# Kernel optimization log

Measured on AMD Instinct MI355X. Metric: run time of the kernel, lower is better.

The kernel has to match this reference:

```python
import jax, jax.numpy as jnp
import numpy as np

V, E, H, B, S, T, NE, NC = 50000, 300, 150, 64, 16, 48, 100001, 300


def bigru(x, Wih, Whh, bih, bhh):
    # x: [T, N, D]; PyTorch GRU cell math, bidirectional -> [T, N, 2H]
    outs = []
    for d in range(2):
        def step(h, xt, d=d):
            gi = xt @ Wih[d].T + bih[d]
            gh = h @ Whh[d].T + bhh[d]
            ir, iz, inn = jnp.split(gi, 3, axis=-1)
            hr, hz, hn = jnp.split(gh, 3, axis=-1)
            r = jax.nn.sigmoid(ir + hr)
            z = jax.nn.sigmoid(iz + hz)
            n = jnp.tanh(inn + r * hn)
            h2 = (1.0 - z) * n + z * h
            return h2, h2
        h0 = jnp.zeros((x.shape[1], Whh.shape[-1]), x.dtype)
        _, hs = jax.lax.scan(step, h0, x, reverse=(d == 1))
        outs.append(hs)
    return jnp.concatenate(outs, axis=-1)


def attend(hs, W, b, ctx):
    # hs: [T, N, G]; softmax attention over time axis
    u = jnp.tanh(jnp.einsum('tng,hg->tnh', hs, W) + b)
    a = jax.nn.softmax(jnp.einsum('tnh,h->tn', u, ctx), axis=0)
    return jnp.einsum('tn,tng->ng', a, hs)


def cos_sim(a, c, eps=1e-8):
    # a: [B, D], c: [B, K, D] -> [B, K]  (torch.cosine_similarity semantics)
    num = jnp.einsum('bd,bkd->bk', a, c)
    den = jnp.linalg.norm(a, axis=-1, keepdims=True) * jnp.linalg.norm(c, axis=-1)
    return num / jnp.maximum(den, eps)


def setup_inputs() -> dict:
    key = jax.random.key(0)
    ks = jax.random.split(key, 20)
    nrm = lambda k, s: (jax.random.normal(k, s, jnp.float32) * 0.05)
    return {
        'docs': jax.random.randint(ks[0], (B, S, T), 0, V),
        'sens': jax.random.randint(ks[1], (B,), 0, S),
        'candidates': jax.random.randint(ks[2], (B, 1, NC), 0, NE),
        'idx': jax.random.randint(ks[3], (B,), 1, NC + 1),  # 1-based gold id
        'word_emb': nrm(ks[4], (V, E)),
        'ent_emb': nrm(ks[5], (NE, E)),
        'Wih_w': nrm(ks[6], (2, 3 * H, E)),
        'Whh_w': nrm(ks[7], (2, 3 * H, H)),
        'bih_w': jnp.zeros((2, 3 * H), jnp.float32),
        'bhh_w': jnp.zeros((2, 3 * H), jnp.float32),
        'attW_w': nrm(ks[8], (2 * H, 2 * H)),
        'attb_w': jnp.zeros((2 * H,), jnp.float32),
        'ctx_w': nrm(ks[9], (2 * H,)),
        'Wih_s': nrm(ks[10], (2, 3 * H, 2 * H)),
        'Whh_s': nrm(ks[11], (2, 3 * H, H)),
        'bih_s': jnp.zeros((2, 3 * H), jnp.float32),
        'bhh_s': jnp.zeros((2, 3 * H), jnp.float32),
        'attW_s': nrm(ks[12], (2 * H, 2 * H)),
        'attb_s': jnp.zeros((2 * H,), jnp.float32),
        'ctx_s': nrm(ks[13], (2 * H,)),
        'linW': nrm(ks[14], (NC, 2 * NC)),
        'linb': jnp.zeros((NC,), jnp.float32),
    }


def reference(docs, sens, candidates, idx, word_emb, ent_emb,
              Wih_w, Whh_w, bih_w, bhh_w, attW_w, attb_w, ctx_w,
              Wih_s, Whh_s, bih_s, bhh_s, attW_s, attb_s, ctx_s,
              linW, linb):
    b, s, t = docs.shape
    # ---- word-level encoder over every sentence at once ----
    x = word_emb[docs]                              # [B,S,T,E]
    x = x.transpose(2, 0, 1, 3).reshape(t, b * s, E)  # [T, B*S, E]
    hs = bigru(x, Wih_w, Whh_w, bih_w, bhh_w)       # [T, B*S, 2H]
    sent_vec = attend(hs, attW_w, attb_w, ctx_w)    # [B*S, 2H]
    sent_vec = sent_vec.reshape(b, s, 2 * H)        # output_per_sen.permute(1,0,2)
    output_sen = sent_vec[jnp.arange(b), sens]      # [B, 2H] mention sentence
    # ---- sentence-level encoder ----
    xs = sent_vec.transpose(1, 0, 2)                # [S, B, 2H]
    hss = bigru(xs, Wih_s, Whh_s, bih_s, bhh_s)     # [S, B, 2H]
    output_doc = attend(hss, attW_s, attb_s, ctx_s)  # [B, 2H]
    # ---- batched cosine similarity against candidate entity embeddings ----
    can = ent_emb[candidates[:, 0]]                 # [B, NC, E]
    sim_total = jnp.concatenate([cos_sim(output_sen, can), cos_sim(output_doc, can)], axis=1)  # [B, 2*NC]
    score = sim_total @ linW.T + linb               # [B, NC]
    score_gold = score[jnp.arange(b), idx - 1]      # [B]
    max_index = jnp.argmax(score, axis=1)           # [B]
    return (score_gold, score, max_index)
```

## Files before the change

### kernel.cpp

```cpp
#include <hip/hip_runtime.h>
#include <hip/hip_bf16.h>
#include <math.h>

#define B_  64
#define S_  16
#define T_  48
#define E_  300
#define H_  150
#define G_  300
#define NC_ 300
#define NW_ (B_*S_)
#define RW_ (T_*NW_)
#define RS_ (S_*B_)
#define GST 960

typedef __attribute__((ext_vector_type(8))) short bf16x8;
typedef __attribute__((ext_vector_type(4))) float f32x4;

__device__ __forceinline__ float sigm(float x){ return 1.0f/(1.0f+__expf(-x)); }

__device__ __forceinline__ ushort f2bf_rne(float x){
  uint u = __float_as_uint(x);
  return (ushort)((u + 0x7FFFu + ((u>>16)&1u)) >> 16);
}

__global__ __launch_bounds__(256) void prep_whh_kernel(
    const float* __restrict__ Whh, float* __restrict__ Wblk){
  int idx = blockIdx.x*256 + threadIdx.x;
  if (idx >= 2*38*450*4) return;
  int k  = idx & 3;
  int j  = (idx >> 2) % 450;
  int e4 = (idx >> 2) / 450 % 38;
  int d  = idx / (38*450*4);
  int e  = e4*4 + k;
  Wblk[idx] = (e < 150) ? Whh[((size_t)d*450 + j)*150 + e] : 0.f;
}

__global__ __launch_bounds__(256) void prep_whh_mfma(
    const float* __restrict__ Whh, ushort* __restrict__ Bsh,
    ushort* __restrict__ Bsl){
  int idx = blockIdx.x*256 + threadIdx.x;
  if (idx >= 2*512*160) return;
  int k = idx % 160;
  int j = (idx / 160) % 512;
  int d = idx / (512*160);
  float x = (j < 450 && k < 150) ? Whh[((size_t)d*450 + j)*150 + k] : 0.f;
  ushort hb = f2bf_rne(x);
  Bsh[idx] = hb;
  Bsl[idx] = f2bf_rne(x - __uint_as_float(((uint)hb)<<16));
}

__global__ __launch_bounds__(128) void split_w_gen(
    const float* __restrict__ W, ushort* __restrict__ Whi,
    ushort* __restrict__ Wlo, int R, int C, int Cp){
  int j = blockIdx.x;
  for (int k = threadIdx.x; k < Cp; k += 128){
    float x = (j < R && k < C) ? W[(size_t)j*C + k] : 0.f;
    ushort hb = f2bf_rne(x);
    float hf = __uint_as_float(((uint)hb)<<16);
    Whi[(size_t)j*Cp + k] = hb;
    Wlo[(size_t)j*Cp + k] = f2bf_rne(x - hf);
  }
}

__global__ __launch_bounds__(256) void gi_mfma_v5(
    const int* __restrict__ docs, const float* __restrict__ emb,
    const ushort* __restrict__ Whi, const ushort* __restrict__ Wlo,
    const float* __restrict__ bih, float* __restrict__ gi){
  __shared__ __align__(16) ushort Bhi[2][16*328];
  __shared__ __align__(16) ushort Blo[2][16*328];
  __shared__ __align__(16) float  Cst[64*36];
  __shared__ int toks[64];
  int tid = threadIdx.x;
  int gr0 = blockIdx.x * 64;
  int t  = gr0 >> 10;
  int n0 = gr0 & 1023;
  if (tid < 64) toks[tid] = docs[(n0 + tid)*T_ + t];
  uint4 pb[5];
#pragma unroll
  for (int i=0;i<5;i++){
    int c = tid + i*256;
    int half = (c >= 640) ? 1 : 0; int cc = c - half*640;
    int row = cc/40, o16 = cc - row*40;
    const ushort* src = half ? Wlo : Whi;
    pb[i] = *(const uint4*)&src[(size_t)row*320 + o16*8];
  }
  __syncthreads();
  int w = tid >> 6, L = tid & 63;
  int lrow = L & 15, lseg = L >> 4;
  const float* aptr = emb + (size_t)toks[w*16 + lrow]*300;
  bf16x8 ah[10], al[10];
#pragma unroll
  for (int ks=0; ks<10; ks++){
    int k0 = ks*32 + lseg*8;
    float x[8];
    if (k0 + 8 <= 300){
      float4 v0 = *(const float4*)&aptr[k0];
      float4 v1 = *(const float4*)&aptr[k0+4];
      x[0]=v0.x; x[1]=v0.y; x[2]=v0.z; x[3]=v0.w;
      x[4]=v1.x; x[5]=v1.y; x[6]=v1.z; x[7]=v1.w;
    } else {
#pragma unroll
      for (int u=0;u<8;u++) x[u] = (k0+u < 300) ? aptr[k0+u] : 0.f;
    }
#pragma unroll
    for (int u=0;u<8;u++){
      ushort hb = f2bf_rne(x[u]);
      float lo = x[u] - __uint_as_float(((uint)hb)<<16);
      ah[ks][u] = (short)hb;
      al[ks][u] = (short)f2bf_rne(lo);
    }
  }
#pragma unroll
  for (int i=0;i<5;i++){
    int c = tid + i*256;
    int half = (c >= 640) ? 1 : 0; int cc = c - half*640;
    int row = cc/40, o16 = cc - row*40;
    ushort* dst = half ? Blo[0] : Bhi[0];
    *(uint4*)&dst[row*328 + o16*8] = pb[i];
  }
  __syncthreads();
  int buf = 0;
  int bfb = lrow*328 + lseg*8;
  int rl0 = w*16 + lseg*4;
  f32x4 acc2[2];
  for (int g2 = 0; g2 < 28; ++g2){
#pragma unroll
    for (int q = 0; q < 2; ++q){
      int nt = g2*2 + q;
#pragma unroll
      for (int i=0;i<5;i++){
        int c = tid + i*256;
        int half = (c >= 640) ? 1 : 0; int cc = c - half*640;
        int row = cc/40, o16 = cc - row*40;
        const ushort* src = half ? Wlo : Whi;
        pb[i] = *(const uint4*)&src[(size_t)((nt+1)*16 + row)*320 + o16*8];
      }
      f32x4 acc = {0.f, 0.f, 0.f, 0.f};
#pragma unroll
      for (int ks=0; ks<10; ks++){
        bf16x8 bh = *(const bf16x8*)&Bhi[buf][bfb + ks*32];
        bf16x8 bl = *(const bf16x8*)&Blo[buf][bfb + ks*32];
        acc = __builtin_amdgcn_mfma_f32_16x16x32_bf16(ah[ks], bh, acc, 0, 0, 0);
        acc = __builtin_amdgcn_mfma_f32_16x16x32_bf16(ah[ks], bl, acc, 0, 0, 0);
        acc = __builtin_amdgcn_mfma_f32_16x16x32_bf16(al[ks], bh, acc, 0, 0, 0);
      }
      acc2[q] = acc;
#pragma unroll
      for (int i=0;i<5;i++){
        int c = tid + i*256;
        int half = (c >= 640) ? 1 : 0; int cc = c - half*640;
        int row = cc/40, o16 = cc - row*40;
        ushort* dst = half ? Blo[buf^1] : Bhi[buf^1];
        *(uint4*)&dst[row*328 + o16*8] = pb[i];
      }
      __syncthreads();
      buf ^= 1;
    }
#pragma unroll
    for (int q = 0; q < 2; ++q){
#pragma unroll
      for (int r = 0; r < 4; ++r)
        Cst[(rl0 + r)*36 + q*16 + lrow] = acc2[q][r];
    }
    __syncthreads();
#pragma unroll
    for (int i = 0; i < 2; ++i){
      int idxc = tid + i*256;
      int row = idxc >> 3, c2 = idxc & 7;
      int colb = g2*32 + c2*4;
      float4 v = *(float4*)&Cst[row*36 + c2*4];
      float4 bb = *(const float4*)&bih[colb];
      v.x += bb.x; v.y += bb.y; v.z += bb.z; v.w += bb.w;
      *(float4*)&gi[(size_t)(gr0 + row)*GST + colb] = v;
    }
  }
  {
    f32x4 acc = {0.f, 0.f, 0.f, 0.f};
#pragma unroll
    for (int ks=0; ks<10; ks++){
      bf16x8 bh = *(const bf16x8*)&Bhi[buf][bfb + ks*32];
      bf16x8 bl = *(const bf16x8*)&Blo[buf][bfb + ks*32];
      acc = __builtin_amdgcn_mfma_f32_16x16x32_bf16(ah[ks], bh, acc, 0, 0, 0);
      acc = __builtin_amdgcn_mfma_f32_16x16x32_bf16(ah[ks], bl, acc, 0, 0, 0);
      acc = __builtin_amdgcn_mfma_f32_16x16x32_bf16(al[ks], bh, acc, 0, 0, 0);
    }
    int col = 896 + lrow;
    if (col < 900){
      float bb = bih[col];
#pragma unroll
      for (int r=0;r<4;r++)
        gi[(size_t)(gr0 + rl0 + r)*GST + col] = acc[r] + bb;
    }
  }
}

__global__ __launch_bounds__(256,3) void att_mfma_kernel(
    const float* __restrict__ hs, const ushort* __restrict__ Whi,
    const ushort* __restrict__ Wlo, const float* __restrict__ bias,
    const float* __restrict__ ctx, float* __restrict__ score, int Rtot){
  __shared__ __align__(16) ushort Bhi[2][16*328];
  __shared__ __align__(16) ushort Blo[2][16*328];
  int tid = threadIdx.x;
  int r0 = blockIdx.x * 64;
  uint4 pb[5];
#pragma unroll
  for (int i=0;i<5;i++){
    int c = tid + i*256;
    int half = (c >= 640) ? 1 : 0; int cc = c - half*640;
    int row = cc/40, o16 = cc - row*40;
    const ushort* src = half ? Wlo : Whi;
    pb[i] = *(const uint4*)&src[(size_t)row*320 + o16*8];
  }
  int w = tid >> 6, L = tid & 63;
  int lrow = L & 15, lseg = L >> 4;
  int arow = r0 + w*16 + lrow;
  bool avalid = arow < Rtot;
  const float* aptr = hs + (size_t)(avalid ? arow : 0)*300;
  bf16x8 ah[10], al[10];
#pragma unroll
  for (int ks=0; ks<10; ks++){
    int k0 = ks*32 + lseg*8;
    float x[8];
    if (avalid && k0 + 8 <= 300){
      float4 v0 = *(const float4*)&aptr[k0];
      float4 v1 = *(const float4*)&aptr[k0+4];
      x[0]=v0.x; x[1]=v0.y; x[2]=v0.z; x[3]=v0.w;
      x[4]=v1.x; x[5]=v1.y; x[6]=v1.z; x[7]=v1.w;
    } else {
#pragma unroll
      for (int u=0;u<8;u++) x[u] = (avalid && k0+u < 300) ? aptr[k0+u] : 0.f;
    }
#pragma unroll
    for (int u=0;u<8;u++){
      ushort hb = f2bf_rne(x[u]);
      float lo = x[u] - __uint_as_float(((uint)hb)<<16);
      ah[ks][u] = (short)hb;
      al[ks][u] = (short)f2bf_rne(lo);
    }
  }
#pragma unroll
  for (int i=0;i<5;i++){
    int c = tid + i*256;
    int half = (c >= 640) ? 1 : 0; int cc = c - half*640;
    int row = cc/40, o16 = cc - row*40;
    ushort* dst = half ? Blo[0] : Bhi[0];
    *(uint4*)&dst[row*328 + o16*8] = pb[i];
  }
  __syncthreads();
  int buf = 0;
  int bfb = lrow*328 + lseg*8;
  float part[4] = {0.f,0.f,0.f,0.f};
  for (int nt = 0; nt < 19; ++nt){
    if (nt < 18){
#pragma unroll
      for (int i=0;i<5;i++){
        int c = tid + i*256;
        int half = (c >= 640) ? 1 : 0; int cc = c - half*640;
        int row = cc/40, o16 = cc - row*40;
        const ushort* src = half ? Wlo : Whi;
        pb[i] = *(const uint4*)&src[(size_t)((nt+1)*16 + row)*320 + o16*8];
      }
    }
    f32x4 acc = {0.f, 0.f, 0.f, 0.f};
#pragma unroll
    for (int ks=0; ks<10; ks++){
      bf16x8 bh = *(const bf16x8*)&Bhi[buf][bfb + ks*32];
      bf16x8 bl = *(const bf16x8*)&Blo[buf][bfb + ks*32];
      acc = __builtin_amdgcn_mfma_f32_16x16x32_bf16(ah[ks], bh, acc, 0, 0, 0);
      acc = __builtin_amdgcn_mfma_f32_16x16x32_bf16(ah[ks], bl, acc, 0, 0, 0);
      acc = __builtin_amdgcn_mfma_f32_16x16x32_bf16(al[ks], bh, acc, 0, 0, 0);
    }
    int col = nt*16 + lrow;
    if (col < 300){
      float bb = bias[col], cx = ctx[col];
#pragma unroll
      for (int r=0;r<4;r++) part[r] += cx * tanhf(acc[r] + bb);
    }
    if (nt < 18){
#pragma unroll
      for (int i=0;i<5;i++){
        int c = tid + i*256;
        int half = (c >= 640) ? 1 : 0; int cc = c - half*640;
        int row = cc/40, o16 = cc - row*40;
        ushort* dst = half ? Blo[buf^1] : Bhi[buf^1];
        *(uint4*)&dst[row*328 + o16*8] = pb[i];
      }
    }
    __syncthreads();
    buf ^= 1;
  }
#pragma unroll
  for (int off=1; off<16; off<<=1){
#pragma unroll
    for (int r=0;r<4;r++) part[r] += __shfl_xor(part[r], off);
  }
  if (lrow == 0){
    int rbase = r0 + w*16 + lseg*4;
#pragma unroll
    for (int r=0;r<4;r++)
      if (rbase + r < Rtot) score[rbase + r] = part[r];
  }
}

__global__ __launch_bounds__(256) void sent_gi_kernel(
    const float* __restrict__ sv, const float* __restrict__ Wih,
    const float* __restrict__ bih, float* __restrict__ gi){
  __shared__ float A[16][G_];
  int r0 = blockIdx.x * 16;
  int s  = r0 >> 6;
  int bb_ = r0 & 63;
  for (int idx = threadIdx.x; idx < 16*75; idx += 256){
    int row = idx / 75, e4 = idx - row*75;
    *(float4*)&A[row][e4*4] =
        *(const float4*)&sv[(((size_t)(bb_+row))*S_ + s)*G_ + e4*4];
  }
  __syncthreads();
  int q = threadIdx.x;
  if (q >= 225) return;
  int j0 = q*4;
  const float4* w0 = (const float4*)(Wih + (size_t)(j0  )*G_);
  const float4* w1 = (const float4*)(Wih + (size_t)(j0+1)*G_);
  const float4* w2 = (const float4*)(Wih + (size_t)(j0+2)*G_);
  const float4* w3 = (const float4*)(Wih + (size_t)(j0+3)*G_);
  float acc[16][4];
#pragma unroll
  for (int i=0;i<16;i++){ acc[i][0]=0.f; acc[i][1]=0.f; acc[i][2]=0.f; acc[i][3]=0.f; }
  for (int e4=0; e4<75; e4++){
    float4 b0=w0[e4], b1=w1[e4], b2=w2[e4], b3=w3[e4];
#pragma unroll
    for (int i=0;i<16;i++){
      float4 av = *(const float4*)&A[i][e4*4];
      acc[i][0] += av.x*b0.x + av.y*b0.y + av.z*b0.z + av.w*b0.w;
      acc[i][1] += av.x*b1.x + av.y*b1.y + av.z*b1.z + av.w*b1.w;
      acc[i][2] += av.x*b2.x + av.y*b2.y + av.z*b2.z + av.w*b2.w;
      acc[i][3] += av.x*b3.x + av.y*b3.y + av.z*b3.z + av.w*b3.w;
    }
  }
  float4 bb = *(const float4*)&bih[j0];
#pragma unroll
  for (int i=0;i<16;i++){
    float4 o4;
    o4.x = acc[i][0]+bb.x; o4.y = acc[i][1]+bb.y;
    o4.z = acc[i][2]+bb.z; o4.w = acc[i][3]+bb.w;
    *(float4*)&gi[((size_t)(s*B_) + bb_ + i)*GST + j0] = o4;
  }
}

__global__ __launch_bounds__(512,2) void gru_mfma2(
    const float* __restrict__ gi, const ushort* __restrict__ Bsh,
    const ushort* __restrict__ Bsl, const float* __restrict__ bhh,
    float* __restrict__ hs, int T, int N){
  __shared__ __align__(16) ushort Ahi[16*168];
  __shared__ __align__(16) ushort Alo[16*168];
  __shared__ float gh[16*468];
  __shared__ float lds_pad[10240];
  int tid = threadIdx.x;
  int d  = blockIdx.y;
  int n0 = blockIdx.x * 8;
  if (N == -12345) lds_pad[tid] = 0.f;
  for (int i = tid; i < 16*168; i += 512){ Ahi[i] = 0; Alo[i] = 0; }
  int wv = tid >> 6, L = tid & 63;
  int lrow = L & 15, lseg = L >> 4;
  bf16x8 Bh[4][5], Bl[4][5];
  {
    const ushort* bh_ = Bsh + (size_t)d*512*160;
    const ushort* bl_ = Bsl + (size_t)d*512*160;
#pragma unroll
    for (int q=0;q<4;q++){
      int row = (wv + q*8)*16 + lrow;
#pragma unroll
      for (int ks=0;ks<5;ks++){
        Bh[q][ks] = *(const bf16x8*)&bh_[(size_t)row*160 + lseg*8 + ks*32];
        Bl[q][ks] = *(const bf16x8*)&bl_[(size_t)row*160 + lseg*8 + ks*32];
      }
    }
  }
  int erow[3], eh[3];
  float bb_r[3], bb_z[3], bb_n[3], hold[3];
#pragma unroll
  for (int r=0;r<3;r++){
    int e = tid + r*512;
    bool v = e < 1200;
    int e2 = v ? e : 0;
    erow[r] = e2 / 150; eh[r] = e2 % 150;
    bb_r[r] = v ? bhh[d*450 + eh[r]]        : 0.f;
    bb_z[r] = v ? bhh[d*450 + 150 + eh[r]]  : 0.f;
    bb_n[r] = v ? bhh[d*450 + 300 + eh[r]]  : 0.f;
    hold[r] = 0.f;
  }
  __syncthreads();
  for (int step = 0; step < T; ++step){
    int t = d ? (T-1-step) : step;
    bf16x8 Ah[5], Al[5];
#pragma unroll
    for (int ks=0;ks<5;ks++){
      Ah[ks] = *(const bf16x8*)&Ahi[lrow*168 + lseg*8 + ks*32];
      Al[ks] = *(const bf16x8*)&Alo[lrow*168 + lseg*8 + ks*32];
    }
#pragma unroll
    for (int q=0;q<4;q++){
      int nt = wv + q*8;
      if (nt < 29){
        f32x4 acc = {0.f,0.f,0.f,0.f};
#pragma unroll
        for (int ks=0;ks<5;ks++){
          acc = __builtin_amdgcn_mfma_f32_16x16x32_bf16(Ah[ks], Bh[q][ks], acc, 0,0,0);
          acc = __builtin_amdgcn_mfma_f32_16x16x32_bf16(Ah[ks], Bl[q][ks], acc, 0,0,0);
          acc = __builtin_amdgcn_mfma_f32_16x16x32_bf16(Al[ks], Bh[q][ks], acc, 0,0,0);
        }
        int col = nt*16 + lrow;
#pragma unroll
        for (int r=0;r<4;r++)
          gh[(lseg*4 + r)*468 + col] = acc[r];
      }
    }
    const float* gib = gi + ((size_t)t*N + n0)*GST + d*450;
    float pr[3], pz[3], pn[3];
#pragma unroll
    for (int r=0;r<3;r++){
      if (tid + r*512 < 1200){
        const float* g0 = gib + (size_t)erow[r]*GST + eh[r];
        pr[r] = g0[0]; pz[r] = g0[150]; pn[r] = g0[300];
      }
    }
    __syncthreads();
#pragma unroll
    for (int r=0;r<3;r++){
      if (tid + r*512 < 1200){
        int row = erow[r], h = eh[r];
        float ghr = gh[row*468 + h];
        float ghz = gh[row*468 + 150 + h];
        float ghn = gh[row*468 + 300 + h];
        float rr = sigm(pr[r] + ghr + bb_r[r]);
        float zz = sigm(pz[r] + ghz + bb_z[r]);
        float nn = tanhf(pn[r] + rr*(ghn + bb_n[r]));
        float h2 = (1.f - zz)*nn + zz*hold[r];
        hold[r] = h2;
        ushort hb = f2bf_rne(h2);
        Ahi[row*168 + h] = hb;
        Alo[row*168 + h] = f2bf_rne(h2 - __uint_as_float(((uint)hb)<<16));
        hs[((size_t)t*N + n0 + row)*G_ + d*H_ + h] = h2;
      }
    }
    __syncthreads();
  }
}

template<int R>
__global__ __launch_bounds__(512,2) void gru_scan_v4(
    const float* __restrict__ gi, const float* __restrict__ Wblk,
    const float* __restrict__ bhh, float* __restrict__ hs,
    int T, int N){
  int d  = blockIdx.y;
  int n0 = blockIdx.x * R;
  __shared__ float hl[2][R][152];
  __shared__ float gh[R][452];
  int tid = threadIdx.x;
  for (int idx = tid; idx < 2*R*152; idx += 512) (&hl[0][0][0])[idx] = 0.f;
  bool jact = tid < 450;
  bool hact = tid < 150;
  float4 Wr[38];
  float bj = 0.f;
  {
    const float4* Wb4 = (const float4*)(Wblk + (size_t)d*38*1800);
    int jj = jact ? tid : 0;
#pragma unroll
    for (int e4 = 0; e4 < 38; ++e4) Wr[e4] = Wb4[e4*450 + jj];
    if (jact) bj = bhh[d*450 + tid];
  }
  float hreg[R];
#pragma unroll
  for (int i=0;i<R;i++) hreg[i] = 0.f;
  int buf = 0;
  __syncthreads();
  for (int step = 0; step < T; ++step){
    int t = d ? (T-1-step) : step;
    const float* gib = gi + ((size_t)t*N + n0)*GST + d*450;
    float pre[R][3];
    if (hact){
#pragma unroll
      for (int i=0;i<R;i++){
        pre[i][0] = gib[(size_t)i*GST + tid];
        pre[i][1] = gib[(size_t)i*GST + 150 + tid];
        pre[i][2] = gib[(size_t)i*GST + 300 + tid];
      }
    }
    if (jact){
      float acc[R];
#pragma unroll
      for (int i=0;i<R;i++) acc[i] = 0.f;
#pragma unroll
      for (int e4 = 0; e4 < 38; ++e4){
        float4 w = Wr[e4];
#pragma unroll
        for (int i=0;i<R;i++){
          float4 hv = *(const float4*)&hl[buf][i][e4*4];
          acc[i] += w.x*hv.x + w.y*hv.y + w.z*hv.z + w.w*hv.w;
        }
      }
#pragma unroll
      for (int i=0;i<R;i++) gh[i][tid] = acc[i] + bj;
    }
    __syncthreads();
    if (hact){
#pragma unroll
      for (int i=0;i<R;i++){
        float r  = sigm(pre[i][0] + gh[i][tid]);
        float z  = sigm(pre[i][1] + gh[i][150+tid]);
        float nn = tanhf(pre[i][2] + r*gh[i][300+tid]);
        float h2 = (1.f - z)*nn + z*hreg[i];
        hreg[i] = h2;
        hl[buf^1][i][tid] = h2;
        hs[((size_t)t*N + n0 + i)*G_ + d*H_ + tid] = h2;
      }
    }
    buf ^= 1;
    __syncthreads();
  }
}

__global__ __launch_bounds__(256) void att_combine_kernel(
    const float* __restrict__ score, const float* __restrict__ hs,
    float* __restrict__ out, int T, int N){
  int n = blockIdx.x;
  __shared__ float wa[64];
  if (threadIdx.x < T) wa[threadIdx.x] = score[threadIdx.x*N + n];
  __syncthreads();
  float m = -1e30f;
  for (int t=0;t<T;t++) m = fmaxf(m, wa[t]);
  float den = 0.f;
  for (int t=0;t<T;t++) den += __expf(wa[t]-m);
  float inv = 1.f/den;
  __syncthreads();
  if (threadIdx.x < T) wa[threadIdx.x] = __expf(wa[threadIdx.x]-m)*inv;
  __syncthreads();
  for (int g = threadIdx.x; g < G_; g += 256){
    float acc = 0.f;
    for (int t=0;t<T;t++) acc += wa[t] * hs[((size_t)t*N+n)*G_ + g];
    out[(size_t)n*G_ + g] = acc;
  }
}

__global__ __launch_bounds__(256) void cossim_kernel(
    const int* __restrict__ cand, const int* __restrict__ sens,
    const float* __restrict__ ent, const float* __restrict__ sv,
    const float* __restrict__ odoc, float* __restrict__ sim){
  int w = (blockIdx.x*256 + threadIdx.x) >> 6;
  int lane = threadIdx.x & 63;
  if (w >= B_*NC_) return;
  int b = w / NC_, k = w - b*NC_;
  const float* c  = ent + (size_t)cand[b*NC_ + k]*E_;
  const float* a1 = sv  + ((size_t)b*S_ + sens[b])*G_;
  const float* a2 = odoc + (size_t)b*G_;
  float d1=0.f,d2=0.f,cc=0.f,n1=0.f,n2=0.f;
  for (int e = lane; e < E_; e += 64){
    float cv=c[e], v1=a1[e], v2=a2[e];
    d1+=v1*cv; d2+=v2*cv; cc+=cv*cv; n1+=v1*v1; n2+=v2*v2;
  }
  for (int off=32; off; off>>=1){
    d1+=__shfl_xor(d1,off); d2+=__shfl_xor(d2,off); cc+=__shfl_xor(cc,off);
    n1+=__shfl_xor(n1,off); n2+=__shfl_xor(n2,off);
  }
  if (lane == 0){
    float nc = sqrtf(cc);
    sim[(size_t)b*600 + k]       = d1 / fmaxf(sqrtf(n1)*nc, 1e-8f);
    sim[(size_t)b*600 + 300 + k] = d2 / fmaxf(sqrtf(n2)*nc, 1e-8f);
  }
}

__global__ __launch_bounds__(256) void final_kernel(
    const float* __restrict__ sim, const float* __restrict__ linW,
    const float* __restrict__ linb, const int* __restrict__ idx,
    float* __restrict__ out){
  int b = blockIdx.x;
  __shared__ float ss[600];
  __shared__ float sc[300];
  __shared__ float bv[256];
  __shared__ int   bi[256];
  for (int j = threadIdx.x; j < 600; j += 256) ss[j] = sim[(size_t)b*600 + j];
  __syncthreads();
  float bestv = -1e30f; int besti = 0;
  for (int i = threadIdx.x; i < 300; i += 256){
    const float4* wr = (const float4*)(linW + (size_t)i*600);
    float acc = linb[i];
    for (int j4=0; j4<150; j4++){
      float4 w = wr[j4];
      int j = j4*4;
      acc += w.x*ss[j] + w.y*ss[j+1] + w.z*ss[j+2] + w.w*ss[j+3];
    }
    sc[i] = acc;
    out[64 + (size_t)b*300 + i] = acc;
    if (acc > bestv){ bestv = acc; besti = i; }
  }
  bv[threadIdx.x] = bestv; bi[threadIdx.x] = besti;
  __syncthreads();
  for (int s=128; s; s>>=1){
    if (threadIdx.x < s){
      float ov = bv[threadIdx.x+s]; int oi = bi[threadIdx.x+s];
      if (ov > bv[threadIdx.x] || (ov == bv[threadIdx.x] && oi < bi[threadIdx.x])){
        bv[threadIdx.x] = ov; bi[threadIdx.x] = oi;
      }
    }
    __syncthreads();
  }
  if (threadIdx.x == 0){
    out[b] = sc[idx[b]-1];
    out[64 + 64*300 + b] = (float)bi[0];
  }
}

extern "C" void kernel_launch(void* const* d_in, const int* in_sizes, int n_in,
                              void* d_out, int out_size, void* d_ws, size_t ws_size,
                              hipStream_t stream){
  const int*   docs  = (const int*)d_in[0];
  const int*   sens  = (const int*)d_in[1];
  const int*   cand  = (const int*)d_in[2];
  const int*   idx   = (const int*)d_in[3];
  const float* wemb  = (const float*)d_in[4];
  const float* eemb  = (const float*)d_in[5];
  const float* Wih_w = (const float*)d_in[6];
  const float* Whh_w = (const float*)d_in[7];
  const float* bih_w = (const float*)d_in[8];
  const float* bhh_w = (const float*)d_in[9];
  const float* attW_w= (const float*)d_in[10];
  const float* attb_w= (const float*)d_in[11];
  const float* ctx_w = (const float*)d_in[12];
  const float* Wih_s = (const float*)d_in[13];
  const float* Whh_s = (const float*)d_in[14];
  const float* bih_s = (const float*)d_in[15];
  const float* bhh_s = (const float*)d_in[16];
  const float* attW_s= (const float*)d_in[17];
  const float* attb_s= (const float*)d_in[18];
  const float* ctx_s = (const float*)d_in[19];
  const float* linW  = (const float*)d_in[20];
  const float* linb  = (const float*)d_in[21];

  float* ws = (float*)d_ws;
  size_t off = 0;
  float* gi_w    = ws + off; off += (size_t)T_*NW_*GST;
  float* hs_w    = ws + off; off += (size_t)T_*NW_*G_;
  float* score_w = ws + off; off += (size_t)T_*NW_;
  float* sv      = ws + off; off += (size_t)NW_*G_;
  float* hs_s    = ws + off; off += (size_t)S_*B_*G_;
  float* score_s = ws + off; off += (size_t)S_*B_;
  float* odoc    = ws + off; off += (size_t)B_*G_;
  float* sim     = ws + off; off += (size_t)B_*600;
  float* Wblk_s  = ws + off; off += (size_t)2*38*450*4;
  ushort* Whi    = (ushort*)(ws + off); off += (size_t)912*320/2;
  ushort* Wlo    = (ushort*)(ws + off); off += (size_t)912*320/2;
  ushort* WAhi   = (ushort*)(ws + off); off += (size_t)304*320/2;
  ushort* WAlo   = (ushort*)(ws + off); off += (size_t)304*320/2;
  ushort* WShi   = (ushort*)(ws + off); off += (size_t)304*320/2;
  ushort* WSlo   = (ushort*)(ws + off); off += (size_t)304*320/2;
  ushort* Bsh    = (ushort*)(ws + off); off += (size_t)2*512*160/2;
  ushort* Bsl    = (ushort*)(ws + off); off += (size_t)2*512*160/2;
  float* gi_s    = gi_w;

  float* out = (float*)d_out;

  prep_whh_kernel<<<(2*38*450*4+255)/256, 256, 0, stream>>>(Whh_s, Wblk_s);
  prep_whh_mfma<<<(2*512*160+255)/256, 256, 0, stream>>>(Whh_w, Bsh, Bsl);
  split_w_gen<<<912, 128, 0, stream>>>(Wih_w, Whi, Wlo, 900, 300, 320);
  split_w_gen<<<304, 128, 0, stream>>>(attW_w, WAhi, WAlo, 300, 300, 320);
  split_w_gen<<<304, 128, 0, stream>>>(attW_s, WShi, WSlo, 300, 300, 320);

  gi_mfma_v5<<<RW_/64, 256, 0, stream>>>(docs, wemb, Whi, Wlo, bih_w, gi_w);
  gru_mfma2<<<dim3(NW_/8, 2), 512, 0, stream>>>(gi_w, Bsh, Bsl, bhh_w,
                                                hs_w, T_, NW_);
  att_mfma_kernel<<<RW_/64, 256, 0, stream>>>(hs_w, WAhi, WAlo, attb_w,
                                              ctx_w, score_w, RW_);
  att_combine_kernel<<<NW_, 256, 0, stream>>>(score_w, hs_w, sv, T_, NW_);

  sent_gi_kernel<<<RS_/16, 256, 0, stream>>>(sv, Wih_s, bih_s, gi_s);
  gru_scan_v4<2><<<dim3(B_/2, 2), 512, 0, stream>>>(gi_s, Wblk_s, bhh_s,
                                                    hs_s, S_, B_);
  att_mfma_kernel<<<RS_/64, 256, 0, stream>>>(hs_s, WShi, WSlo, attb_s,
                                              ctx_s, score_s, RS_);
  att_combine_kernel<<<B_, 256, 0, stream>>>(score_s, hs_s, odoc, S_, B_);

  cossim_kernel<<<(B_*NC_*64)/256, 256, 0, stream>>>(cand, sens, eemb, sv, odoc, sim);
  final_kernel<<<B_, 256, 0, stream>>>(sim, linW, linb, idx, out);
}
```

Measured before the change: 686.9 us.

## Store word-level GRU input gates in MFMA-tile layout, drop LDS staging

The input-gate GEMM now writes its accumulator tiles directly to global memory in a tiled [t][row-block][col-tile][64x16] layout instead of staging through shared memory into a row-major [row][960] array. The GRU scan computes per-thread offsets into this tiled layout to fetch r/z/n gate inputs. This removes the LDS round trip and one barrier per pair of tiles, at the cost of narrower 4-byte strided stores and scattered reads in the recurrence. The workspace buffer is resized to match the tiled layout (57 tiles of 16 columns).

```diff
diff --git a/kernel.cpp b/kernel.cpp
--- a/kernel.cpp
+++ b/kernel.cpp
@@ -63,18 +63,18 @@
   }
 }
 
-__global__ __launch_bounds__(256) void gi_mfma_v5(
+__global__ __launch_bounds__(256) void gi_mfma_v6(
     const int* __restrict__ docs, const float* __restrict__ emb,
     const ushort* __restrict__ Whi, const ushort* __restrict__ Wlo,
-    const float* __restrict__ bih, float* __restrict__ gi){
+    const float* __restrict__ bih, float* __restrict__ giT){
   __shared__ __align__(16) ushort Bhi[2][16*328];
   __shared__ __align__(16) ushort Blo[2][16*328];
-  __shared__ __align__(16) float  Cst[64*36];
   __shared__ int toks[64];
   int tid = threadIdx.x;
   int gr0 = blockIdx.x * 64;
   int t  = gr0 >> 10;
   int n0 = gr0 & 1023;
+  int nblk = n0 >> 6;
   if (tid < 64) toks[tid] = docs[(n0 + tid)*T_ + t];
   uint4 pb[5];
 #pragma unroll
@@ -122,12 +122,10 @@
   __syncthreads();
   int buf = 0;
   int bfb = lrow*328 + lseg*8;
-  int rl0 = w*16 + lseg*4;
-  f32x4 acc2[2];
-  for (int g2 = 0; g2 < 28; ++g2){
-#pragma unroll
-    for (int q = 0; q < 2; ++q){
-      int nt = g2*2 + q;
+  float* tile0 = giT + ((size_t)(t*16 + nblk)*57)*1024
+                     + (w*16 + lseg*4)*16 + lrow;
+  for (int nt = 0; nt < 57; ++nt){
+    if (nt < 56){
 #pragma unroll
       for (int i=0;i<5;i++){
         int c = tid + i*256;
@@ -136,16 +134,24 @@
         const ushort* src = half ? Wlo : Whi;
         pb[i] = *(const uint4*)&src[(size_t)((nt+1)*16 + row)*320 + o16*8];
       }
-      f32x4 acc = {0.f, 0.f, 0.f, 0.f};
-#pragma unroll
-      for (int ks=0; ks<10; ks++){
-        bf16x8 bh = *(const bf16x8*)&Bhi[buf][bfb + ks*32];
-        bf16x8 bl = *(const bf16x8*)&Blo[buf][bfb + ks*32];
-        acc = __builtin_amdgcn_mfma_f32_16x16x32_bf16(ah[ks], bh, acc, 0, 0, 0);
-        acc = __builtin_amdgcn_mfma_f32_16x16x32_bf16(ah[ks], bl, acc, 0, 0, 0);
-        acc = __builtin_amdgcn_mfma_f32_16x16x32_bf16(al[ks], bh, acc, 0, 0, 0);
-      }
-      acc2[q] = acc;
+    }
+    f32x4 acc = {0.f, 0.f, 0.f, 0.f};
+#pragma unroll
+    for (int ks=0; ks<10; ks++){
+      bf16x8 bh = *(const bf16x8*)&Bhi[buf][bfb + ks*32];
+      bf16x8 bl = *(const bf16x8*)&Blo[buf][bfb + ks*32];
+      acc = __builtin_amdgcn_mfma_f32_16x16x32_bf16(ah[ks], bh, acc, 0, 0, 0);
+      acc = __builtin_amdgcn_mfma_f32_16x16x32_bf16(ah[ks], bl, acc, 0, 0, 0);
+      acc = __builtin_amdgcn_mfma_f32_16x16x32_bf16(al[ks], bh, acc, 0, 0, 0);
+    }
+    {
+      int col = nt*16 + lrow;
+      float bb = (col < 900) ? bih[col] : 0.f;
+      float* p = tile0 + (size_t)nt*1024;
+#pragma unroll
+      for (int r=0;r<4;r++) p[r*16] = acc[r] + bb;
+    }
+    if (nt < 56){
 #pragma unroll
       for (int i=0;i<5;i++){
         int c = tid + i*256;
@@ -154,44 +160,9 @@
         ushort* dst = half ? Blo[buf^1] : Bhi[buf^1];
         *(uint4*)&dst[row*328 + o16*8] = pb[i];
       }
-      __syncthreads();
-      buf ^= 1;
-    }
-#pragma unroll
-    for (int q = 0; q < 2; ++q){
-#pragma unroll
-      for (int r = 0; r < 4; ++r)
-        Cst[(rl0 + r)*36 + q*16 + lrow] = acc2[q][r];
     }
     __syncthreads();
-#pragma unroll
-    for (int i = 0; i < 2; ++i){
-      int idxc = tid + i*256;
-      int row = idxc >> 3, c2 = idxc & 7;
-      int colb = g2*32 + c2*4;
-      float4 v = *(float4*)&Cst[row*36 + c2*4];
-      float4 bb = *(const float4*)&bih[colb];
-      v.x += bb.x; v.y += bb.y; v.z += bb.z; v.w += bb.w;
-      *(float4*)&gi[(size_t)(gr0 + row)*GST + colb] = v;
-    }
-  }
-  {
-    f32x4 acc = {0.f, 0.f, 0.f, 0.f};
-#pragma unroll
-    for (int ks=0; ks<10; ks++){
-      bf16x8 bh = *(const bf16x8*)&Bhi[buf][bfb + ks*32];
-      bf16x8 bl = *(const bf16x8*)&Blo[buf][bfb + ks*32];
-      acc = __builtin_amdgcn_mfma_f32_16x16x32_bf16(ah[ks], bh, acc, 0, 0, 0);
-      acc = __builtin_amdgcn_mfma_f32_16x16x32_bf16(ah[ks], bl, acc, 0, 0, 0);
-      acc = __builtin_amdgcn_mfma_f32_16x16x32_bf16(al[ks], bh, acc, 0, 0, 0);
-    }
-    int col = 896 + lrow;
-    if (col < 900){
-      float bb = bih[col];
-#pragma unroll
-      for (int r=0;r<4;r++)
-        gi[(size_t)(gr0 + rl0 + r)*GST + col] = acc[r] + bb;
-    }
+    buf ^= 1;
   }
 }
 
@@ -348,7 +319,7 @@
 }
 
 __global__ __launch_bounds__(512,2) void gru_mfma2(
-    const float* __restrict__ gi, const ushort* __restrict__ Bsh,
+    const float* __restrict__ giT, const ushort* __restrict__ Bsh,
     const ushort* __restrict__ Bsl, const float* __restrict__ bhh,
     float* __restrict__ hs, int T, int N){
   __shared__ __align__(16) ushort Ahi[16*168];
@@ -358,6 +329,7 @@
   int tid = threadIdx.x;
   int d  = blockIdx.y;
   int n0 = blockIdx.x * 8;
+  int nblk = n0 >> 6, rowbase = n0 & 63;
   if (N == -12345) lds_pad[tid] = 0.f;
   for (int i = tid; i < 16*168; i += 512){ Ahi[i] = 0; Alo[i] = 0; }
   int wv = tid >> 6, L = tid & 63;
@@ -378,6 +350,7 @@
   }
   int erow[3], eh[3];
   float bb_r[3], bb_z[3], bb_n[3], hold[3];
+  size_t offr[3], offz[3], offn[3];
 #pragma unroll
   for (int r=0;r<3;r++){
     int e = tid + r*512;
@@ -388,6 +361,13 @@
     bb_z[r] = v ? bhh[d*450 + 150 + eh[r]]  : 0.f;
     bb_n[r] = v ? bhh[d*450 + 300 + eh[r]]  : 0.f;
     hold[r] = 0.f;
+    int cr = d*450 + eh[r];
+    int cz = d*450 + 150 + eh[r];
+    int cn = d*450 + 300 + eh[r];
+    int rw = rowbase + erow[r];
+    offr[r] = (size_t)(cr>>4)*1024 + rw*16 + (cr&15);
+    offz[r] = (size_t)(cz>>4)*1024 + rw*16 + (cz&15);
+    offn[r] = (size_t)(cn>>4)*1024 + rw*16 + (cn&15);
   }
   __syncthreads();
   for (int step = 0; step < T; ++step){
@@ -415,13 +395,14 @@
           gh[(lseg*4 + r)*468 + col] = acc[r];
       }
     }
-    const float* gib = gi + ((size_t)t*N + n0)*GST + d*450;
+    const float* base = giT + ((size_t)(t*16 + nblk)*57)*1024;
     float pr[3], pz[3], pn[3];
 #pragma unroll
     for (int r=0;r<3;r++){
       if (tid + r*512 < 1200){
-        const float* g0 = gib + (size_t)erow[r]*GST + eh[r];
-        pr[r] = g0[0]; pz[r] = g0[150]; pn[r] = g0[300];
+        pr[r] = base[offr[r]];
+        pz[r] = base[offz[r]];
+        pn[r] = base[offn[r]];
       }
     }
     __syncthreads();
@@ -638,7 +619,7 @@
 
   float* ws = (float*)d_ws;
   size_t off = 0;
-  float* gi_w    = ws + off; off += (size_t)T_*NW_*GST;
+  float* gi_w    = ws + off; off += (size_t)T_*16*57*1024;
   float* hs_w    = ws + off; off += (size_t)T_*NW_*G_;
   float* score_w = ws + off; off += (size_t)T_*NW_;
   float* sv      = ws + off; off += (size_t)NW_*G_;
@@ -665,7 +646,7 @@
   split_w_gen<<<304, 128, 0, stream>>>(attW_w, WAhi, WAlo, 300, 300, 320);
   split_w_gen<<<304, 128, 0, stream>>>(attW_s, WShi, WSlo, 300, 300, 320);
 
-  gi_mfma_v5<<<RW_/64, 256, 0, stream>>>(docs, wemb, Whi, Wlo, bih_w, gi_w);
+  gi_mfma_v6<<<RW_/64, 256, 0, stream>>>(docs, wemb, Whi, Wlo, bih_w, gi_w);
   gru_mfma2<<<dim3(NW_/8, 2), 512, 0, stream>>>(gi_w, Bsh, Bsl, bhh_w,
                                                 hs_w, T_, NW_);
   att_mfma_kernel<<<RW_/64, 256, 0, stream>>>(hs_w, WAhi, WAlo, attb_w,
```

Result: slower. 788.1 us (median of 2 runs) (+14.7%).
